# Performance work log

Measured on AMD Instinct MI355X. Metric: run time of the kernel, lower is better.

The kernel has to match this reference:

```python
import jax, jax.numpy as jnp
import numpy as np

NUM_HEADS = 16
WINDOW = 256


def setup_inputs() -> dict:
    key = jax.random.key(0)
    ks = jax.random.split(key, 9)
    B, S, H = 2, 2048, 1024
    sc = 0.02
    return {
        "hidden_states": jax.random.normal(ks[0], (B, S, H), jnp.float32),
        "wq": jax.random.normal(ks[1], (H, H), jnp.float32) * sc,
        "bq": jax.random.normal(ks[2], (H,), jnp.float32) * sc,
        "wk": jax.random.normal(ks[3], (H, H), jnp.float32) * sc,
        "bk": jax.random.normal(ks[4], (H,), jnp.float32) * sc,
        "wv": jax.random.normal(ks[5], (H, H), jnp.float32) * sc,
        "bv": jax.random.normal(ks[6], (H,), jnp.float32) * sc,
        "wo": jax.random.normal(ks[7], (H, H), jnp.float32) * sc,
        "bo": jax.random.normal(ks[8], (H,), jnp.float32) * sc,
    }


def reference(hidden_states, wq, bq, wk, bk, wv, bv, wo, bo):
    B, S, H = hidden_states.shape
    nH, hd = NUM_HEADS, H // NUM_HEADS
    scale = 1.0 / np.sqrt(hd).astype(np.float32)

    def heads(x):  # [B,S,H] -> [B,nH,S,hd]
        return x.reshape(B, S, nH, hd).transpose(0, 2, 1, 3)

    q = heads(hidden_states @ wq.T + bq)
    k = heads(hidden_states @ wk.T + bk)
    v = heads(hidden_states @ wv.T + bv)

    scores = jnp.einsum("bhqd,bhkd->bhqk", q, k) * scale  # [B,nH,S,S]

    # allowed keys for query i: j in [i - WINDOW, i] (causal window)
    i = jnp.arange(S)[:, None]
    j = jnp.arange(S)[None, :]
    allowed = (j <= i) & (j >= i - WINDOW)  # [S,S]

    scores = jnp.where(allowed[None, None], scores, -jnp.inf)
    # original clamps AFTER masking -> -inf becomes -10000 (soft mask)
    scores = jnp.clip(scores, -10000.0, 10000.0)

    probs = jax.nn.softmax(scores, axis=-1)
    probs = jnp.nan_to_num(probs, nan=0.0, posinf=0.0, neginf=0.0)

    out = jnp.einsum("bhqk,bhkd->bhqd", probs, v)  # [B,nH,S,hd]
    out = out.transpose(0, 2, 1, 3).reshape(B, S, H)
    return out @ wo.T + bo
```

## Files before the change

### kernel.cpp

```cpp
#include <hip/hip_runtime.h>
#include <hip/hip_bf16.h>
#include <stdint.h>

typedef __attribute__((ext_vector_type(8))) short short8;
typedef __attribute__((ext_vector_type(4))) float f32x4;
typedef __attribute__((ext_vector_type(4))) unsigned short u16x4;

__device__ __forceinline__ float bf2f(unsigned short u) {
  union { unsigned int u; float f; } x; x.u = ((unsigned int)u) << 16; return x.f;
}
__device__ __forceinline__ unsigned short f2bf(float f) {
  union { float f; unsigned int u; } x; x.f = f;
  unsigned int u = x.u;
  return (unsigned short)((u + 0x7fffu + ((u >> 16) & 1u)) >> 16);
}

__device__ __forceinline__ void gload_lds16(const void* g, void* l) {
  __builtin_amdgcn_global_load_lds(
      (const __attribute__((address_space(1))) void*)g,
      (__attribute__((address_space(3))) void*)l, 16, 0, 0);
}

__global__ void cvt_all(const float* __restrict__ X,
                        const float* __restrict__ w0, const float* __restrict__ w1,
                        const float* __restrict__ w2, const float* __restrict__ w3,
                        unsigned short* __restrict__ Xb,
                        unsigned short* __restrict__ Wb,
                        unsigned short* __restrict__ Ones) {
  if (blockIdx.y == 0) {
    int i = (blockIdx.x * 256 + threadIdx.x) * 4;
    f32x4 f = *(const f32x4*)(X + i);
    u16x4 o = { f2bf(f[0]), f2bf(f[1]), f2bf(f[2]), f2bf(f[3]) };
    *(u16x4*)(Xb + i) = o;
  } else if (blockIdx.y == 1) {
    int wi = blockIdx.x >> 10;
    const float* s = wi == 0 ? w0 : wi == 1 ? w1 : wi == 2 ? w2 : w3;
    int j = ((blockIdx.x & 1023) * 256 + threadIdx.x) * 4;
    f32x4 f = *(const f32x4*)(s + j);
    u16x4 o = { f2bf(f[0]), f2bf(f[1]), f2bf(f[2]), f2bf(f[3]) };
    *(u16x4*)(Wb + ((size_t)wi << 20) + j) = o;
  } else {
    if (blockIdx.x < 32) {
      int j = (blockIdx.x * 256 + threadIdx.x) * 4;
      unsigned short v = (j < 2048) ? (unsigned short)0x3F80 : (unsigned short)0;
      u16x4 o = { v, v, v, v };
      *(u16x4*)(Ones + j) = o;
    }
  }
}

__global__ __launch_bounds__(512, 2)
void gemm_qkv_fused(const unsigned short* __restrict__ A,
                    const unsigned short* __restrict__ Wbase,
                    const float* __restrict__ bq, const float* __restrict__ bk,
                    const float* __restrict__ bv,
                    unsigned short* __restrict__ obf) {
  const int K = 1024, NT = 32;
  constexpr int ASZ = 128 * 32;
  constexpr int BSZ = 3 * 128 * 32;
  __shared__ unsigned short lds[3 * (ASZ + BSZ)];

  int flat = blockIdx.y * 8 + blockIdx.x;
  int swz = (flat & 7) * 32 + (flat >> 3);
  const int n0 = (swz & 7) * 128, m0 = (swz >> 3) * 128;

  const int tid = threadIdx.x, lane = tid & 63, w = tid >> 6;
  const int wr = w >> 1, wc = w & 1;
  const int fr = lane & 15, g = lane >> 4;

  f32x4 acc[3][2][4] = {};

#define STAGE_A(bi, t)                                                          \
  do {                                                                          \
    int s = tid;                                                                \
    int row = s >> 2;                                                           \
    int gc = (s & 3) ^ ((row >> 1) & 3);                                        \
    gload_lds16(A + (size_t)(m0 + row) * K + (t) * 32 + gc * 8,                 \
                &lds[(bi) * (ASZ + BSZ) + s * 8]);                              \
  } while (0)

#define STAGE_W(bi, t, i)                                                       \
  do {                                                                          \
    int s = (i) * 512 + tid;                                                    \
    int row = s >> 2;                                                           \
    int zz = row >> 7, br = row & 127;                                          \
    int gc = (s & 3) ^ ((row >> 1) & 3);                                        \
    gload_lds16(Wbase + ((size_t)zz << 20) + (size_t)(n0 + br) * K +            \
                    (t) * 32 + gc * 8,                                          \
                &lds[(bi) * (ASZ + BSZ) + ASZ + s * 8]);                        \
  } while (0)

  STAGE_A(0, 0); STAGE_W(0, 0, 0); STAGE_W(0, 0, 1); STAGE_W(0, 0, 2);
  STAGE_A(1, 1); STAGE_W(1, 1, 0); STAGE_W(1, 1, 1); STAGE_W(1, 1, 2);

  for (int t = 0; t < NT; ++t) {
    if (t < NT - 1)
      asm volatile("s_waitcnt vmcnt(4)" ::: "memory");
    else
      asm volatile("s_waitcnt vmcnt(0)" ::: "memory");
    __builtin_amdgcn_s_barrier();
    __builtin_amdgcn_sched_barrier(0);

    const int bi = t % 3, bi2 = (t + 2) % 3;
    const bool pf = (t + 2 < NT);
    unsigned short* lb = lds + bi * (ASZ + BSZ);

    if (pf) STAGE_A(bi2, t + 2);

    short8 af[2];
#pragma unroll
    for (int m = 0; m < 2; ++m) {
      int ra = wr * 32 + m * 16 + fr;
      af[m] = *(const short8*)&lb[ra * 32 + ((g ^ ((ra >> 1) & 3)) * 8)];
    }

#pragma unroll
    for (int zz = 0; zz < 3; ++zz) {
      short8 bfr[4];
#pragma unroll
      for (int n = 0; n < 4; ++n) {
        int rb2 = zz * 128 + wc * 64 + n * 16 + fr;
        bfr[n] = *(const short8*)&lb[ASZ + rb2 * 32 + ((g ^ ((rb2 >> 1) & 3)) * 8)];
      }
      if (pf) STAGE_W(bi2, t + 2, zz);
      __builtin_amdgcn_s_setprio(1);
#pragma unroll
      for (int m = 0; m < 2; ++m)
#pragma unroll
        for (int n = 0; n < 4; ++n) {
          if (zz < 2)
            acc[zz][m][n] = __builtin_amdgcn_mfma_f32_16x16x32_bf16(
                bfr[n], af[m], acc[zz][m][n], 0, 0, 0);
          else
            acc[zz][m][n] = __builtin_amdgcn_mfma_f32_16x16x32_bf16(
                af[m], bfr[n], acc[zz][m][n], 0, 0, 0);
        }
      __builtin_amdgcn_s_setprio(0);
    }
  }
#undef STAGE_A
#undef STAGE_W

#pragma unroll
  for (int zz = 0; zz < 2; ++zz) {
    const float* bias = zz == 0 ? bq : bk;
#pragma unroll
    for (int m = 0; m < 2; ++m) {
#pragma unroll
      for (int n = 0; n < 4; ++n) {
        int token = m0 + wr * 32 + m * 16 + fr;
        int col0 = n0 + wc * 64 + n * 16 + g * 4;
        f32x4 bvv = *(const f32x4*)&bias[col0];
        u16x4 pk;
#pragma unroll
        for (int i = 0; i < 4; ++i) pk[i] = f2bf(acc[zz][m][n][i] + bvv[i]);
        int hh = col0 >> 6, d0 = col0 & 63;
        int bb = token >> 11, s0 = token & 2047;
        *(u16x4*)&obf[(((size_t)(zz * 32 + bb * 16 + hh)) * 2048 + s0) * 64 + d0] = pk;
      }
    }
  }
#pragma unroll
  for (int m = 0; m < 2; ++m) {
#pragma unroll
    for (int n = 0; n < 4; ++n) {
      int col = n0 + wc * 64 + n * 16 + fr;
      float bias_v = bv[col];
      int row0 = m0 + wr * 32 + m * 16 + g * 4;
      int hh = col >> 6, d = col & 63;
      int bb = row0 >> 11, s0 = row0 & 2047;
      u16x4 pk;
#pragma unroll
      for (int i = 0; i < 4; ++i) pk[i] = f2bf(acc[2][m][n][i] + bias_v);
      *(u16x4*)&obf[(((size_t)(64 + bb * 16 + hh)) * 64 + d) * 2048 + s0] = pk;
    }
  }
}

__global__ __launch_bounds__(256)
void gemm_oproj(const unsigned short* __restrict__ A,
                const unsigned short* __restrict__ W,
                const float* __restrict__ bias, float* __restrict__ of32) {
  const int K = 1024, NT = 16;
  constexpr int ABUF = 128 * 64;
  constexpr int BBUF = 64 * 64;
  constexpr int BUFSZ = ABUF + BBUF;
  __shared__ unsigned short lds[3 * BUFSZ];

  int flat = blockIdx.y * 16 + blockIdx.x;
  int swz = (flat & 7) * 64 + (flat >> 3);
  const int n0 = (swz & 15) * 64, m0 = (swz >> 4) * 128;

  const int tid = threadIdx.x, lane = tid & 63, w = tid >> 6;
  const int wr = w >> 1, wc = w & 1;
  const int fr = lane & 15, g = lane >> 4;

  f32x4 acc[4][2] = {};

#define STAGE(bi, t)                                                            \
  do {                                                                          \
    unsigned short* lb = lds + (bi) * BUFSZ;                                    \
    _Pragma("unroll") for (int i = 0; i < 4; ++i) {                             \
      int c = i * 256 + tid;                                                    \
      int row = c >> 3;                                                         \
      int ch = (c & 7) ^ (row & 7);                                             \
      gload_lds16(A + (size_t)(m0 + row) * K + (t) * 64 + ch * 8, &lb[c * 8]);  \
    }                                                                           \
    _Pragma("unroll") for (int i = 0; i < 2; ++i) {                             \
      int c = i * 256 + tid;                                                    \
      int row = c >> 3;                                                         \
      int ch = (c & 7) ^ (row & 7);                                             \
      gload_lds16(W + (size_t)(n0 + row) * K + (t) * 64 + ch * 8,               \
                  &lb[ABUF + c * 8]);                                           \
    }                                                                           \
  } while (0)

  STAGE(0, 0);
  STAGE(1, 1);
  for (int t = 0; t < NT; ++t) {
    if (t < NT - 1)
      asm volatile("s_waitcnt vmcnt(6)" ::: "memory");
    else
      asm volatile("s_waitcnt vmcnt(0)" ::: "memory");
    __builtin_amdgcn_s_barrier();
    __builtin_amdgcn_sched_barrier(0);
    if (t + 2 < NT) STAGE((t + 2) % 3, t + 2);

    unsigned short* lb = lds + (t % 3) * BUFSZ;
#pragma unroll
    for (int kk = 0; kk < 2; ++kk) {
      const int kc = kk * 4 + g;
      short8 af[4], bf[2];
#pragma unroll
      for (int m = 0; m < 4; ++m) {
        int ra = wr * 64 + m * 16 + fr;
        af[m] = *(const short8*)&lb[ra * 64 + ((kc ^ (ra & 7)) * 8)];
      }
#pragma unroll
      for (int n = 0; n < 2; ++n) {
        int rb = wc * 32 + n * 16 + fr;
        bf[n] = *(const short8*)&lb[ABUF + rb * 64 + ((kc ^ (rb & 7)) * 8)];
      }
      __builtin_amdgcn_s_setprio(1);
#pragma unroll
      for (int m = 0; m < 4; ++m)
#pragma unroll
        for (int n = 0; n < 2; ++n)
          acc[m][n] = __builtin_amdgcn_mfma_f32_16x16x32_bf16(bf[n], af[m],
                                                              acc[m][n], 0, 0, 0);
      __builtin_amdgcn_s_setprio(0);
    }
  }
#undef STAGE

#pragma unroll
  for (int m = 0; m < 4; ++m) {
#pragma unroll
    for (int n = 0; n < 2; ++n) {
      int token = m0 + wr * 64 + m * 16 + fr;
      int col0 = n0 + wc * 32 + n * 16 + g * 4;
      f32x4 bvv = *(const f32x4*)&bias[col0];
      f32x4 o;
#pragma unroll
      for (int i = 0; i < 4; ++i) o[i] = acc[m][n][i] + bvv[i];
      *(f32x4*)&of32[(size_t)token * 1024 + col0] = o;
    }
  }
}

__global__ __launch_bounds__(256)
void attn_mfma(const unsigned short* __restrict__ QKV,
               const unsigned short* __restrict__ Ones,
               unsigned short* __restrict__ AO) {
  const int S = 2048;
  const int b = blockIdx.z, h = blockIdx.y;
  const int q0 = blockIdx.x * 128;
  const size_t hb = (size_t)(b * 16 + h);
  const unsigned short* Qh = QKV + hb * (S * 64);
  const unsigned short* Kh = QKV + 4194304 + hb * (S * 64);
  const unsigned short* Vt = QKV + 8388608 + hb * (S * 64);

  const int tid = threadIdx.x;
  const int lane = tid & 63, w = tid >> 6;
  const int c = lane & 15, g = lane >> 4;
  const int qw0 = q0 + 32 * w;

  __shared__ unsigned short Plds[4][1024];
  char* Pb = (char*)&Plds[w][0];

  short8 qa[2][2];
#pragma unroll
  for (int mi = 0; mi < 2; ++mi)
#pragma unroll
    for (int cs = 0; cs < 2; ++cs)
      qa[mi][cs] = *(const short8*)(Qh + (size_t)(qw0 + 16 * mi + c) * 64 + 32 * cs + g * 8);

  f32x4 o[2][5] = {};

  int kt0 = qw0 - 256; if (kt0 < 0) kt0 = 0;
  const int ktlast = qw0;

  short8 kf[2][2], vf[5];
#pragma unroll
  for (int ni = 0; ni < 2; ++ni)
#pragma unroll
    for (int cs = 0; cs < 2; ++cs)
      kf[ni][cs] = *(const short8*)(Kh + (size_t)(kt0 + 16 * ni + c) * 64 + 32 * cs + g * 8);
#pragma unroll
  for (int ni = 0; ni < 4; ++ni)
    vf[ni] = *(const short8*)(Vt + (size_t)(16 * ni + c) * 2048 + kt0 + g * 8);
  vf[4] = *(const short8*)(Ones + (size_t)c * 2048 + kt0 + g * 8);

  for (int kt = kt0; kt <= ktlast; kt += 32) {
    const int ktn = (kt + 32 <= ktlast) ? kt + 32 : kt;
    short8 kfn[2][2], vfn[5];
#pragma unroll
    for (int ni = 0; ni < 2; ++ni)
#pragma unroll
      for (int cs = 0; cs < 2; ++cs)
        kfn[ni][cs] = *(const short8*)(Kh + (size_t)(ktn + 16 * ni + c) * 64 + 32 * cs + g * 8);
#pragma unroll
    for (int ni = 0; ni < 4; ++ni)
      vfn[ni] = *(const short8*)(Vt + (size_t)(16 * ni + c) * 2048 + ktn + g * 8);
    vfn[4] = *(const short8*)(Ones + (size_t)c * 2048 + ktn + g * 8);

    f32x4 sA[2][2] = {};
#pragma unroll
    for (int mi = 0; mi < 2; ++mi)
#pragma unroll
      for (int ni = 0; ni < 2; ++ni)
#pragma unroll
        for (int cs = 0; cs < 2; ++cs)
          sA[mi][ni] = __builtin_amdgcn_mfma_f32_16x16x32_bf16(qa[mi][cs], kf[ni][cs],
                                                               sA[mi][ni], 0, 0, 0);

#pragma unroll
    for (int mi = 0; mi < 2; ++mi) {
#pragma unroll
      for (int ni = 0; ni < 2; ++ni) {
#pragma unroll
        for (int r = 0; r < 4; ++r) {
          int q = qw0 + 16 * mi + 4 * g + r;
          int k = kt + 16 * ni + c;
          float p = ((unsigned)(q - k) <= 256u) ? __expf(sA[mi][ni][r] * 0.125f) : 0.f;
          int qloc = 16 * mi + 4 * g + r;
          int xr = (qloc & 12) << 2;
          *(unsigned short*)(Pb + ((qloc * 64 + ni * 32 + c * 2) ^ xr)) = f2bf(p);
        }
      }
    }

#pragma unroll
    for (int mi = 0; mi < 2; ++mi) {
      int qloc = 16 * mi + c;
      short8 pa = *(const short8*)(Pb + ((qloc * 64 + g * 16) ^ ((qloc & 12) << 2)));
#pragma unroll
      for (int ni = 0; ni < 5; ++ni)
        o[mi][ni] = __builtin_amdgcn_mfma_f32_16x16x32_bf16(pa, vf[ni], o[mi][ni], 0, 0, 0);
    }

#pragma unroll
    for (int ni = 0; ni < 2; ++ni)
#pragma unroll
      for (int cs = 0; cs < 2; ++cs)
        kf[ni][cs] = kfn[ni][cs];
#pragma unroll
    for (int ni = 0; ni < 5; ++ni)
      vf[ni] = vfn[ni];
  }

#pragma unroll
  for (int mi = 0; mi < 2; ++mi)
#pragma unroll
    for (int r = 0; r < 4; ++r) {
      float ls = __shfl(o[mi][4][r], lane & 48);
      float inv = 1.f / ls;
      int q = qw0 + 16 * mi + 4 * g + r;
      unsigned short* row = AO + (size_t)(b * 2048 + q) * 1024 + h * 64 + c;
#pragma unroll
      for (int ni = 0; ni < 4; ++ni)
        row[16 * ni] = f2bf(o[mi][ni][r] * inv);
    }
}

extern "C" void kernel_launch(void* const* d_in, const int* in_sizes, int n_in,
                              void* d_out, int out_size, void* d_ws, size_t ws_size,
                              hipStream_t stream) {
  const float* X  = (const float*)d_in[0];
  const float* wq = (const float*)d_in[1];
  const float* bq = (const float*)d_in[2];
  const float* wk = (const float*)d_in[3];
  const float* bk = (const float*)d_in[4];
  const float* wv = (const float*)d_in[5];
  const float* bv = (const float*)d_in[6];
  const float* wo = (const float*)d_in[7];
  const float* bo = (const float*)d_in[8];
  float* out = (float*)d_out;

  unsigned short* Xb   = (unsigned short*)d_ws;
  unsigned short* Wb   = Xb + 4194304;
  unsigned short* QKV  = Wb + 4194304;
  unsigned short* AO   = QKV + 12582912;
  unsigned short* Ones = AO + 4194304;

  cvt_all<<<dim3(4096, 3), dim3(256), 0, stream>>>(X, wq, wk, wv, wo, Xb, Wb, Ones);
  gemm_qkv_fused<<<dim3(8, 32), dim3(512), 0, stream>>>(Xb, Wb, bq, bk, bv, QKV);
  attn_mfma<<<dim3(16, 16, 2), dim3(256), 0, stream>>>(QKV, Ones, AO);
  gemm_oproj<<<dim3(16, 32), dim3(256), 0, stream>>>(AO, Wb + 3 * 1048576, bo, out);
}
```

Measured before the change: 84.81 us.

## Remap QKV GEMM warps to 2x4 grid with 64x96 per-warp tiles

Changes the fused QKV GEMM wave layout from 4x2 waves, each covering 32 rows by 64 columns of each of Q, K and V, to 2x4 waves, each covering 64 rows by a 96-column slice of the concatenated 384-column output. Each wave now loads 4 A fragments and 6 B fragments per k-step instead of 2 A and 12 B, cutting LDS reads per MFMA. The cost is that the V epilogue now writes scalar bf16 values into the transposed layout, where it previously wrote packed 4-element vectors, so global stores become less coalesced.

```diff
diff --git a/kernel.cpp b/kernel.cpp
--- a/kernel.cpp
+++ b/kernel.cpp
@@ -65,10 +65,10 @@
   const int n0 = (swz & 7) * 128, m0 = (swz >> 3) * 128;
 
   const int tid = threadIdx.x, lane = tid & 63, w = tid >> 6;
-  const int wr = w >> 1, wc = w & 1;
+  const int wr = w >> 2, wc = w & 3;
   const int fr = lane & 15, g = lane >> 4;
 
-  f32x4 acc[3][2][4] = {};
+  f32x4 acc[4][6] = {};
 
 #define STAGE_A(bi, t)                                                          \
   do {                                                                          \
@@ -107,72 +107,60 @@
 
     if (pf) STAGE_A(bi2, t + 2);
 
-    short8 af[2];
-#pragma unroll
-    for (int m = 0; m < 2; ++m) {
-      int ra = wr * 32 + m * 16 + fr;
+    short8 af[4];
+#pragma unroll
+    for (int m = 0; m < 4; ++m) {
+      int ra = wr * 64 + m * 16 + fr;
       af[m] = *(const short8*)&lb[ra * 32 + ((g ^ ((ra >> 1) & 3)) * 8)];
     }
-
-#pragma unroll
-    for (int zz = 0; zz < 3; ++zz) {
-      short8 bfr[4];
-#pragma unroll
-      for (int n = 0; n < 4; ++n) {
-        int rb2 = zz * 128 + wc * 64 + n * 16 + fr;
-        bfr[n] = *(const short8*)&lb[ASZ + rb2 * 32 + ((g ^ ((rb2 >> 1) & 3)) * 8)];
-      }
-      if (pf) STAGE_W(bi2, t + 2, zz);
-      __builtin_amdgcn_s_setprio(1);
-#pragma unroll
-      for (int m = 0; m < 2; ++m)
-#pragma unroll
-        for (int n = 0; n < 4; ++n) {
-          if (zz < 2)
-            acc[zz][m][n] = __builtin_amdgcn_mfma_f32_16x16x32_bf16(
-                bfr[n], af[m], acc[zz][m][n], 0, 0, 0);
-          else
-            acc[zz][m][n] = __builtin_amdgcn_mfma_f32_16x16x32_bf16(
-                af[m], bfr[n], acc[zz][m][n], 0, 0, 0);
-        }
-      __builtin_amdgcn_s_setprio(0);
-    }
+    short8 bfr[6];
+#pragma unroll
+    for (int n = 0; n < 6; ++n) {
+      int rb2 = wc * 96 + n * 16 + fr;
+      bfr[n] = *(const short8*)&lb[ASZ + rb2 * 32 + ((g ^ ((rb2 >> 1) & 3)) * 8)];
+    }
+    if (pf) { STAGE_W(bi2, t + 2, 0); STAGE_W(bi2, t + 2, 1); STAGE_W(bi2, t + 2, 2); }
+
+    __builtin_amdgcn_s_setprio(1);
+#pragma unroll
+    for (int n = 0; n < 6; ++n)
+#pragma unroll
+      for (int m = 0; m < 4; ++m)
+        acc[m][n] = __builtin_amdgcn_mfma_f32_16x16x32_bf16(bfr[n], af[m],
+                                                            acc[m][n], 0, 0, 0);
+    __builtin_amdgcn_s_setprio(0);
   }
 #undef STAGE_A
 #undef STAGE_W
 
 #pragma unroll
-  for (int zz = 0; zz < 2; ++zz) {
-    const float* bias = zz == 0 ? bq : bk;
-#pragma unroll
-    for (int m = 0; m < 2; ++m) {
-#pragma unroll
-      for (int n = 0; n < 4; ++n) {
-        int token = m0 + wr * 32 + m * 16 + fr;
-        int col0 = n0 + wc * 64 + n * 16 + g * 4;
+  for (int m = 0; m < 4; ++m) {
+#pragma unroll
+    for (int n = 0; n < 6; ++n) {
+      int base = wc * 96 + n * 16;
+      int zz = base >> 7, brb = base & 127;
+      int token = m0 + wr * 64 + m * 16 + fr;
+      int bb = token >> 11, s0 = token & 2047;
+      if (zz < 2) {
+        int col0 = n0 + brb + g * 4;
+        const float* bias = zz ? bk : bq;
         f32x4 bvv = *(const f32x4*)&bias[col0];
         u16x4 pk;
 #pragma unroll
-        for (int i = 0; i < 4; ++i) pk[i] = f2bf(acc[zz][m][n][i] + bvv[i]);
+        for (int i = 0; i < 4; ++i) pk[i] = f2bf(acc[m][n][i] + bvv[i]);
         int hh = col0 >> 6, d0 = col0 & 63;
-        int bb = token >> 11, s0 = token & 2047;
         *(u16x4*)&obf[(((size_t)(zz * 32 + bb * 16 + hh)) * 2048 + s0) * 64 + d0] = pk;
+      } else {
+        int col0 = n0 + brb + g * 4;
+        f32x4 bvv = *(const f32x4*)&bv[col0];
+#pragma unroll
+        for (int i = 0; i < 4; ++i) {
+          int col = col0 + i;
+          int hh = col >> 6, d = col & 63;
+          obf[(((size_t)(64 + bb * 16 + hh)) * 64 + d) * 2048 + s0] =
+              f2bf(acc[m][n][i] + bvv[i]);
+        }
       }
-    }
-  }
-#pragma unroll
-  for (int m = 0; m < 2; ++m) {
-#pragma unroll
-    for (int n = 0; n < 4; ++n) {
-      int col = n0 + wc * 64 + n * 16 + fr;
-      float bias_v = bv[col];
-      int row0 = m0 + wr * 32 + m * 16 + g * 4;
-      int hh = col >> 6, d = col & 63;
-      int bb = row0 >> 11, s0 = row0 & 2047;
-      u16x4 pk;
-#pragma unroll
-      for (int i = 0; i < 4; ++i) pk[i] = f2bf(acc[2][m][n][i] + bias_v);
-      *(u16x4*)&obf[(((size_t)(64 + bb * 16 + hh)) * 64 + d) * 2048 + s0] = pk;
     }
   }
 }
```

Result: slower. 86.59 us (+2.1%).
